# Kernel optimization log

Hardware: AMD Instinct MI355X
Metric: run time of the kernel (lower is better)

The kernel has to match this reference:

```python
import jax, jax.numpy as jnp
import numpy as np
import math

N, C_S, C_Z, C_IPA, H, NQ, NV = 768, 384, 128, 16, 12, 4, 8


def setup_inputs() -> dict:
    key = jax.random.key(0)
    ks = jax.random.split(key, 16)
    inp = {
        "s": jax.random.normal(ks[0], (N, C_S), jnp.float32),
        "z": jax.random.normal(ks[1], (N, N, C_Z), jnp.float32),
        "rots": jax.random.normal(ks[2], (N, 3, 3), jnp.float32),
        "trans": jax.random.normal(ks[3], (N, 3), jnp.float32),
        "mask": jnp.ones((N,), jnp.float32),
    }
    sc = 0.02
    inp["Wq"] = jax.random.normal(ks[4], (C_S, H * C_IPA), jnp.float32) * sc
    inp["bq"] = jnp.zeros((H * C_IPA,), jnp.float32)
    inp["Wkv"] = jax.random.normal(ks[5], (C_S, H * 2 * C_IPA), jnp.float32) * sc
    inp["bkv"] = jnp.zeros((H * 2 * C_IPA,), jnp.float32)
    inp["Wq3"] = jax.random.normal(ks[6], (C_S, H * 3 * NQ), jnp.float32) * sc
    inp["bq3"] = jnp.zeros((H * 3 * NQ,), jnp.float32)
    inp["Wkv3"] = jax.random.normal(ks[7], (C_S, H * 3 * (NQ + NV)), jnp.float32) * sc
    inp["bkv3"] = jnp.zeros((H * 3 * (NQ + NV),), jnp.float32)
    inp["Wb"] = jax.random.normal(ks[8], (C_Z, H), jnp.float32) * sc
    inp["bb"] = jnp.zeros((H,), jnp.float32)
    inp["hw"] = jnp.zeros((H,), jnp.float32)
    inp["Wo"] = jax.random.normal(ks[9], (H * (C_Z + C_IPA + NV * 4), C_S), jnp.float32) * sc
    inp["bo"] = jnp.zeros((C_S,), jnp.float32)
    return inp


def reference(s, z, rots, trans, mask, Wq, bq, Wkv, bkv, Wq3, bq3, Wkv3, bkv3, Wb, bb, hw, Wo, bo):
    normsize = math.sqrt(1.0 / (3 * C_IPA))
    normsize_B = math.sqrt(1.0 / 3.0)
    normsize_hw = math.sqrt(1.0 / (3 * NQ * 9.0 / 2))

    # scalar Q/K/V: [N, H, C_IPA]
    Q = (s @ Wq + bq).reshape(N, H, C_IPA)
    KV = (s @ Wkv + bkv).reshape(N, H, 2, C_IPA)
    K, V = KV[..., 0, :], KV[..., 1, :]

    # query points: project, place into global frame via rigid transform
    Q3 = (s @ Wq3 + bq3).reshape(N, 3, NQ * H).swapaxes(-1, -2)        # [N, NQ*H, 3]
    Q3 = jnp.einsum('nij,nkj->nki', rots, Q3) + trans[:, None, :]
    Q3 = Q3.reshape(N, H, NQ, 3)

    KV3 = (s @ Wkv3 + bkv3).reshape(N, 3, H * (NQ + NV)).swapaxes(-1, -2)
    KV3 = jnp.einsum('nij,nkj->nki', rots, KV3) + trans[:, None, :]
    KV3 = KV3.reshape(N, H, NQ + NV, 3)
    K3, V3 = KV3[:, :, :NQ, :], KV3[:, :, NQ:, :]                      # points per head

    # pair bias [N, N, H]
    B = z @ Wb + bb

    # scalar attention logits + pair bias
    AT = jnp.einsum('ihc,jhc->ijh', Q, K) * normsize + B * normsize_B

    # point attention: squared distances [N, N, H, NQ]
    d2 = jnp.sum(jnp.square(Q3[:, None] - K3[None, :]), axis=-1)
    hw_sp = jax.nn.softplus(hw) * normsize_hw                          # [H]
    AT3 = -0.5 * jnp.sum(d2 * hw_sp[None, None, :, None], axis=-1)     # [N, N, H]

    # mask bias: large negative where either residue masked out
    mask2 = mask[:, None] * mask[None, :]
    B3 = (mask2 - 1.0) * 1e9                                           # [N, N]

    AT = jax.nn.softmax(AT + AT3 + B3[..., None], axis=-2)             # softmax over j

    # scalar value aggregation
    O = jnp.einsum('ijh,jhc->ihc', AT, V).reshape(N, -1)

    # point value aggregation, then map back to local frame (inverse transform)
    O3 = jnp.einsum('ijh,jhcd->ihcd', AT, V3).reshape(N, H * NV, 3)
    O3 = jnp.einsum('nji,nkj->nki', rots, O3 - trans[:, None, :])      # rots^T @ (O3 - t)
    O3_norm = jnp.sqrt(jnp.sum(jnp.square(O3), axis=-1) + 1e-20)       # [N, H*NV]

    # pair representation aggregation
    O_pair = jnp.einsum('ijh,ijc->ihc', AT, z).reshape(N, -1)

    O_final = jnp.concatenate((O, O3[..., 0], O3[..., 1], O3[..., 2], O3_norm, O_pair), axis=-1)
    return O_final @ Wo + bo
```

## Files before the change

### kernel.cpp

```cpp
#include <hip/hip_runtime.h>
#include <cstdint>


typedef __attribute__((ext_vector_type(8))) short short8;
typedef __attribute__((ext_vector_type(4))) short short4_t;
typedef __attribute__((ext_vector_type(4))) float f32x4;

__device__ __forceinline__ unsigned short f2bf(float f) {
    unsigned u = __float_as_uint(f);
    u = (u + 0x7FFFu + ((u >> 16) & 1u)) >> 16;
    return (unsigned short)u;
}
__device__ __forceinline__ float bf2f(unsigned short s) {
    return __uint_as_float(((unsigned)s) << 16);
}
__device__ __forceinline__ unsigned pk2(float lo, float hi) {
    return (unsigned)f2bf(lo) | ((unsigned)f2bf(hi) << 16);
}
__device__ __forceinline__ int HOFF(int gg) {
    return gg * 6 + ((gg & 2) << 2);
}

__global__ __launch_bounds__(256) void proj_kernel(
    const float* __restrict__ s,
    const float* __restrict__ Wq,   const float* __restrict__ bq,
    const float* __restrict__ Wkv,  const float* __restrict__ bkv,
    const float* __restrict__ Wq3,  const float* __restrict__ bq3,
    const float* __restrict__ Wkv3, const float* __restrict__ bkv3,
    float* __restrict__ Qw, unsigned short* __restrict__ Kw,
    unsigned short* __restrict__ Vw,
    float* __restrict__ P3q, float* __restrict__ P3kv)
{
    __shared__ __align__(16) float s_lds[32 * 384];
    const int t  = threadIdx.x;
    const int r0 = blockIdx.x * 32;
    const int c0 = blockIdx.y * 128;

    for (int u = t; u < 3072; u += 256) {
        int r = u / 96, c4 = u - r * 96;
        *(float4*)&s_lds[r * 384 + c4 * 4] =
            *(const float4*)&s[(size_t)(r0 + r) * 384 + c4 * 4];
    }
    __syncthreads();

    const int rg = t >> 6;
    const int lc = t & 63;
    const int colA = c0 + lc;
    const int colB = c0 + lc + 64;

    const float *wpA, *wpB; int ldA, ldB; float biasA, biasB;
    {
        int col = colA;
        if (col < 192)      { wpA = Wq   + col;       ldA = 192; biasA = bq[col]; }
        else if (col < 576) { wpA = Wkv  + (col-192); ldA = 384; biasA = bkv[col-192]; }
        else if (col < 720) { wpA = Wq3  + (col-576); ldA = 144; biasA = bq3[col-576]; }
        else                { wpA = Wkv3 + (col-720); ldA = 432; biasA = bkv3[col-720]; }
        col = colB;
        if (col < 192)      { wpB = Wq   + col;       ldB = 192; biasB = bq[col]; }
        else if (col < 576) { wpB = Wkv  + (col-192); ldB = 384; biasB = bkv[col-192]; }
        else if (col < 720) { wpB = Wq3  + (col-576); ldB = 144; biasB = bq3[col-576]; }
        else                { wpB = Wkv3 + (col-720); ldB = 432; biasB = bkv3[col-720]; }
    }

    float acc0[8] = {}, acc1[8] = {};
    for (int k = 0; k < 384; k += 4) {
        float4 sv[8];
        #pragma unroll
        for (int r = 0; r < 8; r++)
            sv[r] = *(const float4*)&s_lds[(rg*8 + r) * 384 + k];
        #pragma unroll
        for (int kk = 0; kk < 4; kk++) {
            float w0 = wpA[(k + kk) * ldA];
            float w1 = wpB[(k + kk) * ldB];
            #pragma unroll
            for (int r = 0; r < 8; r++) {
                float sval = ((const float*)&sv[r])[kk];
                acc0[r] += sval * w0;
                acc1[r] += sval * w1;
            }
        }
    }

    #pragma unroll
    for (int q = 0; q < 2; q++) {
        int col   = q ? colB : colA;
        float bia = q ? biasB : biasA;
        #pragma unroll
        for (int r = 0; r < 8; r++) {
            int row = r0 + rg*8 + r;
            float v = (q ? acc1[r] : acc0[r]) + bia;
            if (col < 192) {
                Qw[(size_t)row*192 + col] = v;
            } else if (col < 576) {
                int c = col - 192, h = c >> 5, sub = c & 31;
                if (sub < 16) Kw[(size_t)row*192 + h*16 + sub]      = f2bf(v);
                else          Vw[(size_t)row*192 + h*16 + (sub-16)] = f2bf(v);
            } else if (col < 720) {
                P3q[(size_t)row*144 + (col-576)] = v;
            } else {
                P3kv[(size_t)row*432 + (col-720)] = v;
            }
        }
    }
}

__global__ __launch_bounds__(192) void rot3_kernel(
    const float* __restrict__ P3q, const float* __restrict__ P3kv,
    const float* __restrict__ rots, const float* __restrict__ trans,
    float* __restrict__ Q3w, unsigned short* __restrict__ K3w,
    unsigned short* __restrict__ V3w)
{
    const int n = blockIdx.x;
    const int t = threadIdx.x;
    float R[9];
    #pragma unroll
    for (int u = 0; u < 9; u++) R[u] = rots[n*9 + u];
    float T0 = trans[n*3+0], T1 = trans[n*3+1], T2 = trans[n*3+2];

    float p0, p1, p2;
    if (t < 48) {
        p0 = P3q[(size_t)n*144 + t];
        p1 = P3q[(size_t)n*144 + 48 + t];
        p2 = P3q[(size_t)n*144 + 96 + t];
    } else {
        int k = t - 48;
        p0 = P3kv[(size_t)n*432 + k];
        p1 = P3kv[(size_t)n*432 + 144 + k];
        p2 = P3kv[(size_t)n*432 + 288 + k];
    }
    float o0 = R[0]*p0 + R[1]*p1 + R[2]*p2 + T0;
    float o1 = R[3]*p0 + R[4]*p1 + R[5]*p2 + T1;
    float o2 = R[6]*p0 + R[7]*p1 + R[8]*p2 + T2;

    if (t < 48) {
        Q3w[(size_t)n*144 + t*3 + 0] = o0;
        Q3w[(size_t)n*144 + t*3 + 1] = o1;
        Q3w[(size_t)n*144 + t*3 + 2] = o2;
    } else {
        int k = t - 48, h = k / 12, m = k % 12;
        if (m < 4) {
            size_t base = (size_t)n*144 + (h*4 + m)*3;
            K3w[base+0] = f2bf(o0); K3w[base+1] = f2bf(o1); K3w[base+2] = f2bf(o2);
        } else {
            size_t base = (size_t)n*384 + (h*8 + (m-4))*4;
            V3w[base+0] = f2bf(o0); V3w[base+1] = f2bf(o1); V3w[base+2] = f2bf(o2);
        }
    }
}

__global__ __launch_bounds__(256, 4) void ipa_main(
    const float* __restrict__ z, const float* __restrict__ mask,
    const float* __restrict__ Wb, const float* __restrict__ bb,
    const float* __restrict__ hw,
    const float* __restrict__ Qw, const unsigned short* __restrict__ Kw,
    const unsigned short* __restrict__ Vw,
    const float* __restrict__ Q3w, const unsigned short* __restrict__ K3w,
    const unsigned short* __restrict__ V3w,
    float* __restrict__ part3)
{
    __shared__ __align__(16) unsigned short z_l[90 * 88];
    __shared__ __align__(16) unsigned short wbT_l[16 * 136];
    __shared__ __align__(16) float          p_l[32 * 17];
    __shared__ __align__(16) unsigned short pT_l[16 * 40];
    __shared__ __align__(16) float          Q_lds[12 * 17];
    __shared__ __align__(16) float          Q3_lds[12 * 13];
    __shared__ float hw_lds[12], bb_lds[12];

    const int i     = blockIdx.x >> 1;
    const int chunk = blockIdx.x & 1;
    const int t    = threadIdx.x;
    const int lane = t & 63;
    const int wv   = t >> 6;
    const int g    = lane >> 4;
    const int lm   = lane & 15;

    if (t < 192) Q_lds[(t >> 4)*17 + (t & 15)] = Qw[(size_t)i*192 + t];
    if (t < 144) Q3_lds[(t / 12)*13 + (t % 12)] = Q3w[(size_t)i*144 + t];
    if (t < 12) {
        hw_lds[t] = log1pf(__expf(hw[t])) * 0.13608276348795434f;
        bb_lds[t] = bb[t];
    }
    if (t < 160) pT_l[480 + t] = 0;
    for (int u = t; u < 1536; u += 256) {
        int h = u % 12, c = u / 12;
        wbT_l[h*136 + c] = f2bf(Wb[c*12 + h]);
    }
    const float mask_i = mask[i];

    f32x4 opA = {0,0,0,0}, opB = {0,0,0,0};
    float oacc = 0.0f;
    float o3x = 0, o3y = 0, o3z = 0;
    float dena = 0;
    const int oh = t >> 4, oc = t & 15;
    int o3h = -1, o3v = 0, o3j0 = 0, o3j1 = 32, o3slot = 0;
    if (t >= 192)    { o3h = (t - 192) >> 3;      o3v = (t - 192) & 7; }
    else if (t < 32) { o3h = 8 + (t >> 3);        o3v = t & 7;        o3j1 = 16; }
    else if (t < 64) { o3h = 8 + ((t - 32) >> 3); o3v = (t - 32) & 7; o3j0 = 16; o3slot = 1; }
    const int denh = (t >= 64 && t < 76) ? (t - 64) : -1;

    const int jj  = t >> 3, c16 = t & 7;
    const float* zbase = z + ((size_t)i*768 + chunk*384 + jj)*128 + c16*16;
    const int chS  = (jj >> 2)*8 + c16;
    const int chP  = chS + HOFF(chS >> 4);
    const int sidx = chP*88 + (jj & 3)*16;

    __syncthreads();

    for (int tile = 0; tile < 12; tile++) {
        const int j0 = chunk*384 + tile*32;

        {
            const float* zp = zbase + (size_t)tile * 32 * 128;
            float4 f0 = *(const float4*)(zp + 0);
            float4 f1 = *(const float4*)(zp + 4);
            float4 f2 = *(const float4*)(zp + 8);
            float4 f3 = *(const float4*)(zp + 12);
            uint4* dst = (uint4*)&z_l[sidx];
            dst[0] = uint4{pk2(f0.x,f0.y), pk2(f0.z,f0.w), pk2(f1.x,f1.y), pk2(f1.z,f1.w)};
            dst[1] = uint4{pk2(f2.x,f2.y), pk2(f2.z,f2.w), pk2(f3.x,f3.y), pk2(f3.z,f3.w)};
        }
        __syncthreads();

        if (wv < 2) {
            f32x4 ab = {0,0,0,0};
            const int jt = wv;
            #pragma unroll
            for (int ks = 0; ks < 4; ks++) {
                short8 bf = *(const short8*)&wbT_l[lm*136 + ks*32 + g*8];
                int jr = jt*16 + lm;
                int ch = (jr >> 2)*8 + ks*2 + (g >> 1);
                int cp = ch + HOFF(ch >> 4);
                short8 a = *(const short8*)&z_l[cp*88 + (jr & 3)*16 + (g & 1)*8];
                ab = __builtin_amdgcn_mfma_f32_16x16x32_bf16(a, bf, ab, 0, 0, 0);
            }
            if (lm < 12) {
                #pragma unroll
                for (int r = 0; r < 4; r++)
                    p_l[(jt*16 + g*4 + r)*17 + lm] = ab[r];
            }
        }
        __syncthreads();

        {
            auto b2item = [&](int pr) {
                int jjq = pr / 12;
                int h   = pr - jjq*12;
                int j   = j0 + jjq;
                float Bv = p_l[jjq*17 + h];
                const unsigned short* kp = Kw + (size_t)j*192 + h*16;
                short8 kA = *(const short8*)(kp);
                short8 kB = *(const short8*)(kp + 8);
                float qk = 0.0f;
                #pragma unroll
                for (int e = 0; e < 8; e++) qk += Q_lds[h*17 + e]     * bf2f((unsigned short)kA[e]);
                #pragma unroll
                for (int e = 0; e < 8; e++) qk += Q_lds[h*17 + 8 + e] * bf2f((unsigned short)kB[e]);
                const unsigned short* k3p = K3w + (size_t)j*144 + h*12;
                short4_t c0v = *(const short4_t*)(k3p);
                short4_t c1v = *(const short4_t*)(k3p + 4);
                short4_t c2v = *(const short4_t*)(k3p + 8);
                float d2 = 0.0f;
                #pragma unroll
                for (int e = 0; e < 4; e++) { float d = Q3_lds[h*13 + e]     - bf2f((unsigned short)c0v[e]); d2 += d*d; }
                #pragma unroll
                for (int e = 0; e < 4; e++) { float d = Q3_lds[h*13 + 4 + e] - bf2f((unsigned short)c1v[e]); d2 += d*d; }
                #pragma unroll
                for (int e = 0; e < 4; e++) { float d = Q3_lds[h*13 + 8 + e] - bf2f((unsigned short)c2v[e]); d2 += d*d; }
                float mj = mask[j];
                float lg = qk * 0.14433756729740643f
                         + (Bv + bb_lds[h]) * 0.5773502691896258f
                         - 0.5f * hw_lds[h] * d2
                         + (mask_i * mj - 1.0f) * 1e9f;
                float p = __expf(lg);
                p_l[jjq*17 + h]  = p;
                pT_l[h*40 + jjq] = f2bf(p);
            };
            b2item(t);
            if (t >= 128) b2item(t + 128);
        }
        __syncthreads();

        {
            const int nt0 = wv*2;
            short8 ap = *(const short8*)((const char*)pT_l + lm*80 + g*16);
            short8 b0, b1;
            #pragma unroll
            for (int e = 0; e < 8; e++) {
                int jje = g*8 + e;
                int su  = (jje >> 2)*8;
                int ro  = (jje & 3)*16;
                int cp0 = su + nt0 + HOFF(g);
                b0[e] = (short)z_l[cp0*88 + ro + lm];
                b1[e] = (short)z_l[(cp0 + 1)*88 + ro + lm];
            }
            opA = __builtin_amdgcn_mfma_f32_16x16x32_bf16(ap, b0, opA, 0, 0, 0);
            opB = __builtin_amdgcn_mfma_f32_16x16x32_bf16(ap, b1, opB, 0, 0, 0);
        }
        if (t < 192) {
            #pragma unroll 8
            for (int jjq = 0; jjq < 32; jjq++) {
                float p = p_l[jjq*17 + oh];
                oacc += p * bf2f(Vw[(size_t)(j0 + jjq)*192 + oh*16 + oc]);
            }
        }
        if (o3h >= 0) {
            #pragma unroll 8
            for (int jjq = o3j0; jjq < o3j1; jjq++) {
                float p = p_l[jjq*17 + o3h];
                short4_t v4 = *(const short4_t*)(V3w + (size_t)(j0 + jjq)*384 + (o3h*8 + o3v)*4);
                o3x += p * bf2f((unsigned short)v4[0]);
                o3y += p * bf2f((unsigned short)v4[1]);
                o3z += p * bf2f((unsigned short)v4[2]);
            }
        }
        if (denh >= 0) {
            #pragma unroll 8
            for (int jjq = 0; jjq < 32; jjq++) dena += p_l[jjq*17 + denh];
        }
        __syncthreads();
    }

    float* pb = part3 + (size_t)blockIdx.x * 2560;
    if (t < 192) pb[t] = oacc;
    if (o3h >= 0) {
        int base = 192 + o3slot*288 + (o3h*8 + o3v)*3;
        pb[base+0] = o3x; pb[base+1] = o3y; pb[base+2] = o3z;
    }
    if (denh >= 0) pb[2304 + denh] = dena;
    {
        const int nt0 = wv*2;
        #pragma unroll
        for (int r = 0; r < 4; r++) {
            int h = g*4 + r;
            if (h < 12) {
                pb[768 + h*128 + nt0*16 + lm]       = opA[r];
                pb[768 + h*128 + (nt0 + 1)*16 + lm] = opB[r];
            }
        }
    }
}

__global__ __launch_bounds__(256) void combine_kernel(
    const float* __restrict__ part3, const float* __restrict__ rots,
    const float* __restrict__ trans, unsigned short* __restrict__ OF)
{
    const int i = blockIdx.x;
    const int t = threadIdx.x;
    const float* pa = part3 + (size_t)i*2*2560;
    const float* pb = pa + 2560;
    __shared__ float den_s[12];
    if (t < 12) den_s[t] = pa[2304 + t] + pb[2304 + t];
    __syncthreads();

    const size_t ofb = (size_t)i * 2112;
    if (t < 192) OF[ofb + t] = f2bf((pa[t] + pb[t]) / den_s[t >> 4]);
    if (t < 96) {
        int h = t >> 3, v = t & 7;
        float den = den_s[h];
        int base = 192 + t*3;
        float m0 = pa[base+0] + pb[base+0];
        float m1 = pa[base+1] + pb[base+1];
        float m2 = pa[base+2] + pb[base+2];
        if (h >= 8) {
            m0 += pa[base+288+0] + pb[base+288+0];
            m1 += pa[base+288+1] + pb[base+288+1];
            m2 += pa[base+288+2] + pb[base+288+2];
        }
        m0 = m0 / den - trans[i*3+0];
        m1 = m1 / den - trans[i*3+1];
        m2 = m2 / den - trans[i*3+2];
        const float* R = rots + (size_t)i*9;
        float r0v = R[0]*m0 + R[3]*m1 + R[6]*m2;
        float r1v = R[1]*m0 + R[4]*m1 + R[7]*m2;
        float r2v = R[2]*m0 + R[5]*m1 + R[8]*m2;
        float nrm = sqrtf(r0v*r0v + r1v*r1v + r2v*r2v + 1e-20f);
        int hv = h*8 + v;
        OF[ofb + 192 + hv] = f2bf(r0v);
        OF[ofb + 288 + hv] = f2bf(r1v);
        OF[ofb + 384 + hv] = f2bf(r2v);
        OF[ofb + 480 + hv] = f2bf(nrm);
    }
    for (int u = t; u < 1536; u += 256) {
        OF[ofb + 576 + u] = f2bf((pa[768 + u] + pb[768 + u]) / den_s[u >> 7]);
    }
}

__global__ __launch_bounds__(256) void wot_kernel(
    const float* __restrict__ Wo, unsigned short* __restrict__ WoT)
{
    int id = blockIdx.x * 256 + threadIdx.x;
    int c  = id % 384;
    int k8 = id / 384;
    unsigned short tmp[8];
    #pragma unroll
    for (int e = 0; e < 8; e++)
        tmp[e] = f2bf(Wo[(size_t)(k8*8 + e)*384 + c]);
    uint4 o;
    o.x = (unsigned)tmp[0] | ((unsigned)tmp[1] << 16);
    o.y = (unsigned)tmp[2] | ((unsigned)tmp[3] << 16);
    o.z = (unsigned)tmp[4] | ((unsigned)tmp[5] << 16);
    o.w = (unsigned)tmp[6] | ((unsigned)tmp[7] << 16);
    *(uint4*)&WoT[(size_t)c*2112 + k8*8] = o;
}

__global__ __launch_bounds__(256) void out_gemm2(
    const unsigned short* __restrict__ OF, const unsigned short* __restrict__ WoT,
    const float* __restrict__ bo, float* __restrict__ out)
{
    __shared__ __align__(16) unsigned short aT[32 * 72];
    __shared__ __align__(16) unsigned short bT[128 * 72];
    const int t = threadIdx.x;
    const int wv = t >> 6, lane = t & 63, g = lane >> 4, lm = lane & 15;
    const int i0 = blockIdx.x * 32;
    const int c0 = blockIdx.y * 128;

    f32x4 acc00 = {0,0,0,0}, acc01 = {0,0,0,0};
    f32x4 acc10 = {0,0,0,0}, acc11 = {0,0,0,0};

    const int sr = t >> 3, sc = (t & 7) * 8;

    for (int k0 = 0; k0 < 2112; k0 += 64) {
        __syncthreads();
        *(uint4*)&aT[sr*72 + sc] =
            *(const uint4*)&OF[(size_t)(i0 + sr)*2112 + k0 + sc];
        #pragma unroll
        for (int q = 0; q < 4; q++) {
            int br = q*32 + sr;
            *(uint4*)&bT[br*72 + sc] =
                *(const uint4*)&WoT[(size_t)(c0 + br)*2112 + k0 + sc];
        }
        __syncthreads();
        #pragma unroll
        for (int kk = 0; kk < 2; kk++) {
            short8 a0 = *(const short8*)&aT[lm*72        + kk*32 + g*8];
            short8 a1 = *(const short8*)&aT[(16+lm)*72   + kk*32 + g*8];
            short8 b0 = *(const short8*)&bT[(wv*32+lm)*72    + kk*32 + g*8];
            short8 b1 = *(const short8*)&bT[(wv*32+16+lm)*72 + kk*32 + g*8];
            acc00 = __builtin_amdgcn_mfma_f32_16x16x32_bf16(a0, b0, acc00, 0, 0, 0);
            acc01 = __builtin_amdgcn_mfma_f32_16x16x32_bf16(a0, b1, acc01, 0, 0, 0);
            acc10 = __builtin_amdgcn_mfma_f32_16x16x32_bf16(a1, b0, acc10, 0, 0, 0);
            acc11 = __builtin_amdgcn_mfma_f32_16x16x32_bf16(a1, b1, acc11, 0, 0, 0);
        }
    }

    const int colA = c0 + wv*32 + lm, colB = colA + 16;
    const float bA = bo[colA], bB = bo[colB];
    #pragma unroll
    for (int r = 0; r < 4; r++) {
        int rowA = i0 + g*4 + r;
        int rowB = rowA + 16;
        out[(size_t)rowA*384 + colA] = acc00[r] + bA;
        out[(size_t)rowA*384 + colB] = acc01[r] + bB;
        out[(size_t)rowB*384 + colA] = acc10[r] + bA;
        out[(size_t)rowB*384 + colB] = acc11[r] + bB;
    }
}

extern "C" void kernel_launch(void* const* d_in, const int* in_sizes, int n_in,
                              void* d_out, int out_size, void* d_ws, size_t ws_size,
                              hipStream_t stream) {
    const float* s     = (const float*)d_in[0];
    const float* z     = (const float*)d_in[1];
    const float* rots  = (const float*)d_in[2];
    const float* trans = (const float*)d_in[3];
    const float* mask  = (const float*)d_in[4];
    const float* Wq    = (const float*)d_in[5];
    const float* bq    = (const float*)d_in[6];
    const float* Wkv   = (const float*)d_in[7];
    const float* bkv   = (const float*)d_in[8];
    const float* Wq3   = (const float*)d_in[9];
    const float* bq3   = (const float*)d_in[10];
    const float* Wkv3  = (const float*)d_in[11];
    const float* bkv3  = (const float*)d_in[12];
    const float* Wb    = (const float*)d_in[13];
    const float* bb    = (const float*)d_in[14];
    const float* hw    = (const float*)d_in[15];
    const float* Wo    = (const float*)d_in[16];
    const float* bo    = (const float*)d_in[17];
    float* out = (float*)d_out;

    char* ws = (char*)d_ws;
    float*          Qw   = (float*)(ws + 0);
    float*          Q3w  = (float*)(ws + 589824);
    unsigned short* Kw   = (unsigned short*)(ws + 1032192);
    unsigned short* Vw   = (unsigned short*)(ws + 1327104);
    unsigned short* K3w  = (unsigned short*)(ws + 1622016);
    unsigned short* V3w  = (unsigned short*)(ws + 1843200);
    float*          P3q  = (float*)(ws + 2433024);
    float*          P3kv = (float*)(ws + 2875392);
    unsigned short* OF   = (unsigned short*)(ws + 4202496);
    float*          part3 = (float*)(ws + 7446528);
    unsigned short* WoT  = (unsigned short*)(ws + 23175168);

    wot_kernel<<<396, 256, 0, stream>>>(Wo, WoT);
    proj_kernel<<<dim3(24, 9), 256, 0, stream>>>(
        s, Wq, bq, Wkv, bkv, Wq3, bq3, Wkv3, bkv3, Qw, Kw, Vw, P3q, P3kv);
    rot3_kernel<<<768, 192, 0, stream>>>(P3q, P3kv, rots, trans, Q3w, K3w, V3w);
    ipa_main<<<1536, 256, 0, stream>>>(
        z, mask, Wb, bb, hw, Qw, Kw, Vw, Q3w, K3w, V3w, part3);
    combine_kernel<<<768, 256, 0, stream>>>(part3, rots, trans, OF);
    out_gemm2<<<dim3(24, 3), 256, 0, stream>>>(OF, WoT, bo, out);
}
```

Before: 264.1 us.

## Transpose V and V3 to j-contiguous layout and stagger tile order per block

The scalar and point value tensors are now stored transposed, with the key index j contiguous. This lets the aggregation loops in the main attention kernel load 8 consecutive bf16 values per thread with one 16-byte load instead of doing scalar or 4-element strided loads. The j-tile loop order is also rotated by block index, so concurrent blocks read different V tiles and avoid all hitting the same addresses at once. The softmax-item lambda is replaced by an unrolled two-rep loop. The transposed writes in proj_kernel and rot3_kernel become strided scattered stores, which could cost some time in those small kernels.

```diff
diff --git a/kernel.cpp b/kernel.cpp
--- a/kernel.cpp
+++ b/kernel.cpp
@@ -28,7 +28,7 @@
     const float* __restrict__ Wq3,  const float* __restrict__ bq3,
     const float* __restrict__ Wkv3, const float* __restrict__ bkv3,
     float* __restrict__ Qw, unsigned short* __restrict__ Kw,
-    unsigned short* __restrict__ Vw,
+    unsigned short* __restrict__ Vt,
     float* __restrict__ P3q, float* __restrict__ P3kv)
 {
     __shared__ __align__(16) float s_lds[32 * 384];
@@ -93,8 +93,8 @@
                 Qw[(size_t)row*192 + col] = v;
             } else if (col < 576) {
                 int c = col - 192, h = c >> 5, sub = c & 31;
-                if (sub < 16) Kw[(size_t)row*192 + h*16 + sub]      = f2bf(v);
-                else          Vw[(size_t)row*192 + h*16 + (sub-16)] = f2bf(v);
+                if (sub < 16) Kw[(size_t)row*192 + h*16 + sub] = f2bf(v);
+                else          Vt[(size_t)(h*16 + (sub-16))*768 + row] = f2bf(v);
             } else if (col < 720) {
                 P3q[(size_t)row*144 + (col-576)] = v;
             } else {
@@ -108,7 +108,7 @@
     const float* __restrict__ P3q, const float* __restrict__ P3kv,
     const float* __restrict__ rots, const float* __restrict__ trans,
     float* __restrict__ Q3w, unsigned short* __restrict__ K3w,
-    unsigned short* __restrict__ V3w)
+    unsigned short* __restrict__ V3t)
 {
     const int n = blockIdx.x;
     const int t = threadIdx.x;
@@ -142,8 +142,10 @@
             size_t base = (size_t)n*144 + (h*4 + m)*3;
             K3w[base+0] = f2bf(o0); K3w[base+1] = f2bf(o1); K3w[base+2] = f2bf(o2);
         } else {
-            size_t base = (size_t)n*384 + (h*8 + (m-4))*4;
-            V3w[base+0] = f2bf(o0); V3w[base+1] = f2bf(o1); V3w[base+2] = f2bf(o2);
+            int rv = (h*8 + (m-4))*3;
+            V3t[(size_t)(rv+0)*768 + n] = f2bf(o0);
+            V3t[(size_t)(rv+1)*768 + n] = f2bf(o1);
+            V3t[(size_t)(rv+2)*768 + n] = f2bf(o2);
         }
     }
 }
@@ -153,9 +155,9 @@
     const float* __restrict__ Wb, const float* __restrict__ bb,
     const float* __restrict__ hw,
     const float* __restrict__ Qw, const unsigned short* __restrict__ Kw,
-    const unsigned short* __restrict__ Vw,
+    const unsigned short* __restrict__ Vt,
     const float* __restrict__ Q3w, const unsigned short* __restrict__ K3w,
-    const unsigned short* __restrict__ V3w,
+    const unsigned short* __restrict__ V3t,
     float* __restrict__ part3)
 {
     __shared__ __align__(16) unsigned short z_l[90 * 88];
@@ -191,7 +193,7 @@
     float oacc = 0.0f;
     float o3x = 0, o3y = 0, o3z = 0;
     float dena = 0;
-    const int oh = t >> 4, oc = t & 15;
+    const int oh = t >> 4;
     int o3h = -1, o3v = 0, o3j0 = 0, o3j1 = 32, o3slot = 0;
     if (t >= 192)    { o3h = (t - 192) >> 3;      o3v = (t - 192) & 7; }
     else if (t < 32) { o3h = 8 + (t >> 3);        o3v = t & 7;        o3j1 = 16; }
@@ -204,9 +206,12 @@
     const int chP  = chS + HOFF(chS >> 4);
     const int sidx = chP*88 + (jj & 3)*16;
 
+    const int rot = blockIdx.x % 12;
+
     __syncthreads();
 
-    for (int tile = 0; tile < 12; tile++) {
+    for (int tt = 0; tt < 12; tt++) {
+        int tile = tt + rot; if (tile >= 12) tile -= 12;
         const int j0 = chunk*384 + tile*32;
 
         {
@@ -241,8 +246,10 @@
         }
         __syncthreads();
 
-        {
-            auto b2item = [&](int pr) {
+        #pragma unroll
+        for (int rep = 0; rep < 2; rep++) {
+            int pr = t + rep*256;
+            if (pr < 384) {
                 int jjq = pr / 12;
                 int h   = pr - jjq*12;
                 int j   = j0 + jjq;
@@ -274,9 +281,7 @@
                 float p = __expf(lg);
                 p_l[jjq*17 + h]  = p;
                 pT_l[h*40 + jjq] = f2bf(p);
-            };
-            b2item(t);
-            if (t >= 128) b2item(t + 128);
+            }
         }
         __syncthreads();
 
@@ -297,20 +302,29 @@
             opB = __builtin_amdgcn_mfma_f32_16x16x32_bf16(ap, b1, opB, 0, 0, 0);
         }
         if (t < 192) {
-            #pragma unroll 8
-            for (int jjq = 0; jjq < 32; jjq++) {
-                float p = p_l[jjq*17 + oh];
-                oacc += p * bf2f(Vw[(size_t)(j0 + jjq)*192 + oh*16 + oc]);
+            const unsigned short* vp = Vt + (size_t)t*768 + j0;
+            #pragma unroll
+            for (int q = 0; q < 4; q++) {
+                short8 va = *(const short8*)(vp + q*8);
+                #pragma unroll
+                for (int e = 0; e < 8; e++)
+                    oacc += p_l[(q*8 + e)*17 + oh] * bf2f((unsigned short)va[e]);
             }
         }
         if (o3h >= 0) {
-            #pragma unroll 8
-            for (int jjq = o3j0; jjq < o3j1; jjq++) {
-                float p = p_l[jjq*17 + o3h];
-                short4_t v4 = *(const short4_t*)(V3w + (size_t)(j0 + jjq)*384 + (o3h*8 + o3v)*4);
-                o3x += p * bf2f((unsigned short)v4[0]);
-                o3y += p * bf2f((unsigned short)v4[1]);
-                o3z += p * bf2f((unsigned short)v4[2]);
+            const unsigned short* v3p = V3t + (size_t)((o3h*8 + o3v)*3)*768 + j0;
+            #pragma unroll
+            for (int q = o3j0 >> 3; q < (o3j1 >> 3); q++) {
+                short8 vx = *(const short8*)(v3p + q*8);
+                short8 vy = *(const short8*)(v3p + 768 + q*8);
+                short8 vz = *(const short8*)(v3p + 1536 + q*8);
+                #pragma unroll
+                for (int e = 0; e < 8; e++) {
+                    float p = p_l[(q*8 + e)*17 + o3h];
+                    o3x += p * bf2f((unsigned short)vx[e]);
+                    o3y += p * bf2f((unsigned short)vy[e]);
+                    o3z += p * bf2f((unsigned short)vz[e]);
+                }
             }
         }
         if (denh >= 0) {
@@ -483,9 +497,9 @@
     float*          Qw   = (float*)(ws + 0);
     float*          Q3w  = (float*)(ws + 589824);
     unsigned short* Kw   = (unsigned short*)(ws + 1032192);
-    unsigned short* Vw   = (unsigned short*)(ws + 1327104);
+    unsigned short* Vt   = (unsigned short*)(ws + 1327104);
     unsigned short* K3w  = (unsigned short*)(ws + 1622016);
-    unsigned short* V3w  = (unsigned short*)(ws + 1843200);
+    unsigned short* V3t  = (unsigned short*)(ws + 1843200);
     float*          P3q  = (float*)(ws + 2433024);
     float*          P3kv = (float*)(ws + 2875392);
     unsigned short* OF   = (unsigned short*)(ws + 4202496);
@@ -494,10 +508,10 @@
 
     wot_kernel<<<396, 256, 0, stream>>>(Wo, WoT);
     proj_kernel<<<dim3(24, 9), 256, 0, stream>>>(
-        s, Wq, bq, Wkv, bkv, Wq3, bq3, Wkv3, bkv3, Qw, Kw, Vw, P3q, P3kv);
-    rot3_kernel<<<768, 192, 0, stream>>>(P3q, P3kv, rots, trans, Q3w, K3w, V3w);
+        s, Wq, bq, Wkv, bkv, Wq3, bq3, Wkv3, bkv3, Qw, Kw, Vt, P3q, P3kv);
+    rot3_kernel<<<768, 192, 0, stream>>>(P3q, P3kv, rots, trans, Q3w, K3w, V3t);
     ipa_main<<<1536, 256, 0, stream>>>(
-        z, mask, Wb, bb, hw, Qw, Kw, Vw, Q3w, K3w, V3w, part3);
+        z, mask, Wb, bb, hw, Qw, Kw, Vt, Q3w, K3w, V3t, part3);
     combine_kernel<<<768, 256, 0, stream>>>(part3, rots, trans, OF);
     out_gemm2<<<dim3(24, 3), 256, 0, stream>>>(OF, WoT, bo, out);
 }
```

Result: slower. 317.9 us (+20.4%).
